# Kernel tuning notes

Hardware: AMD Instinct MI355X
Metric: run time of the kernel (lower is better)

The kernel has to match this reference:

```python
import jax, jax.numpy as jnp
import numpy as np

NEG_SLOPE = 0.2  # PyG GATConv default


def add_self_loops(edge_index, num_nodes):
    loops = jnp.arange(num_nodes, dtype=edge_index.dtype)
    return jnp.concatenate([edge_index, jnp.stack([loops, loops])], axis=1)


def gat_conv(x, edge_index, W, att_src, att_dst, bias, heads, out_ch, concat):
    # x: [N, F_in]; edge_index: [2, E] with row0=src(j), row1=dst(i)
    N = x.shape[0]
    xl = (x @ W).reshape(N, heads, out_ch)              # [N, H, C]
    src, dst = edge_index[0], edge_index[1]
    a_src = jnp.einsum('nhc,hc->nh', xl, att_src)        # [N, H]
    a_dst = jnp.einsum('nhc,hc->nh', xl, att_dst)        # [N, H]
    alpha = jax.nn.leaky_relu(a_src[src] + a_dst[dst], NEG_SLOPE)  # [E, H]
    # segment softmax over incoming edges of each dst node
    m = jax.ops.segment_max(alpha, dst, num_segments=N)  # [N, H]
    e = jnp.exp(alpha - m[dst])
    denom = jax.ops.segment_sum(e, dst, num_segments=N)
    coef = e / (denom[dst] + 1e-16)                      # [E, H]
    msg = xl[src] * coef[..., None]                      # [E, H, C]
    out = jax.ops.segment_sum(msg, dst, num_segments=N)  # [N, H, C]
    out = out.reshape(N, heads * out_ch) if concat else out.mean(axis=1)
    return out + bias


def setup_inputs() -> dict:
    key = jax.random.key(0)
    ks = jax.random.split(key, 12)
    N, E = 50000, 800000
    nfeat, nhid, nheads, nclass = 512, 8, 8, 16
    hid = nhid * nheads  # 64
    s1 = 1.0 / np.sqrt(nfeat)
    s2 = 1.0 / np.sqrt(hid)
    return {
        'x': jax.random.normal(ks[0], (N, nfeat), jnp.float32),
        'edge_index': jax.random.randint(ks[1], (2, E), 0, N, jnp.int64 if jax.config.jax_enable_x64 else jnp.int32),
        'W1': jax.random.uniform(ks[2], (nfeat, hid), jnp.float32, -s1, s1),
        'att_src1': jax.random.uniform(ks[3], (nheads, nhid), jnp.float32, -s2, s2),
        'att_dst1': jax.random.uniform(ks[4], (nheads, nhid), jnp.float32, -s2, s2),
        'bias1': jnp.zeros((hid,), jnp.float32),
        'W2': jax.random.uniform(ks[5], (hid, nclass), jnp.float32, -s2, s2),
        'att_src2': jax.random.uniform(ks[6], (1, nclass), jnp.float32, -0.25, 0.25),
        'att_dst2': jax.random.uniform(ks[7], (1, nclass), jnp.float32, -0.25, 0.25),
        'bias2': jnp.zeros((nclass,), jnp.float32),
    }


def reference(x, edge_index, W1, att_src1, att_dst1, bias1, W2, att_src2, att_dst2, bias2):
    N = x.shape[0]
    ei = add_self_loops(edge_index, N)
    # dropout layers are identity at inference
    h = gat_conv(x, ei, W1, att_src1, att_dst1, bias1, heads=8, out_ch=8, concat=True)
    o = gat_conv(h, ei, W2, att_src2, att_dst2, bias2, heads=1, out_ch=16, concat=True)
    o = jax.nn.elu(o)
    return jax.nn.log_softmax(o, axis=1)
```

## Files before the change

### kernel.cpp

```cpp
#include <hip/hip_runtime.h>
#include <math.h>

#define NEG_SLOPE 0.2f

typedef short short8 __attribute__((ext_vector_type(8)));
typedef float floatx4 __attribute__((ext_vector_type(4)));

static __device__ __forceinline__ float bf2f(unsigned short u) {
  return __uint_as_float(((unsigned int)u) << 16);
}
static __device__ __forceinline__ unsigned short f2bf(float f) {
  unsigned int u = __float_as_uint(f);
  u = (u + 0x7fffu + ((u >> 16) & 1u)) >> 16;
  return (unsigned short)u;
}

__global__ void init_misc(const float* __restrict__ W1, unsigned short* __restrict__ W1t,
                          int* __restrict__ deg, int N) {
  int b = blockIdx.x;
  if (b < 128) {
    int i = b * 256 + threadIdx.x;
    int k = i >> 6, c = i & 63;
    W1t[c * 512 + k] = f2bf(W1[i]);
  } else {
    int n = (b - 128) * 256 + threadIdx.x;
    if (n < N) deg[n] = 1;
  }
}

__global__ __launch_bounds__(256) void cvt_hist(const float* __restrict__ x,
                                                unsigned short* __restrict__ xb,
                                                const int* __restrict__ ei,
                                                int* __restrict__ deg,
                                                int* __restrict__ rank,
                                                long long total, int E, int ipc, int NH) {
  int b = blockIdx.x;
  int tid = threadIdx.x;
  if (b < NH) {
    int beg = b * ipc;
    int end = min(beg + ipc, E);
    for (int i = beg + tid; i < end; i += 256) {
      int d = ei[E + i];
      rank[i] = atomicAdd(&deg[d], 1);
    }
    return;
  }
  long long base = (long long)(b - NH) * 2048;
  long long i0 = base + tid * 4;
  long long i1 = base + 1024 + tid * 4;
  if (i1 + 4 <= total) {
    float4 f0 = *(const float4*)(x + i0);
    float4 f1 = *(const float4*)(x + i1);
    ushort4 u0 = make_ushort4(f2bf(f0.x), f2bf(f0.y), f2bf(f0.z), f2bf(f0.w));
    ushort4 u1 = make_ushort4(f2bf(f1.x), f2bf(f1.y), f2bf(f1.z), f2bf(f1.w));
    *(ushort4*)(xb + i0) = u0;
    *(ushort4*)(xb + i1) = u1;
  } else {
#pragma unroll
    for (int k = 0; k < 4; ++k) {
      if (i0 + k < total) xb[i0 + k] = f2bf(x[i0 + k]);
      if (i1 + k < total) xb[i1 + k] = f2bf(x[i1 + k]);
    }
  }
}

__global__ __launch_bounds__(256) void gemm1_scan(const unsigned short* __restrict__ xb,
                                                  const unsigned short* __restrict__ W1t,
                                                  const float* __restrict__ att_src,
                                                  const float* __restrict__ att_dst,
                                                  unsigned short* __restrict__ xlb,
                                                  float* __restrict__ a_src,
                                                  float* __restrict__ a_dst, int M,
                                                  const int* __restrict__ deg,
                                                  int* __restrict__ rowptr, int G1) {
  __shared__ unsigned short As[64 * 72];
  __shared__ unsigned short Bs[64 * 72];
  int tid = threadIdx.x;
  if ((int)blockIdx.x >= G1) {
    int* wsum = (int*)As;
    int lane = tid & 63, wv = tid >> 6;
    int carry = 0;
    for (int base = 0; base < M; base += 8192) {
      int i0 = base + tid * 32;
      int d[32];
      if (i0 + 32 <= M) {
#pragma unroll
        for (int g = 0; g < 8; ++g) {
          int4 a = *(const int4*)(deg + i0 + g * 4);
          d[g * 4] = a.x; d[g * 4 + 1] = a.y; d[g * 4 + 2] = a.z; d[g * 4 + 3] = a.w;
        }
      } else {
#pragma unroll
        for (int k = 0; k < 32; ++k) d[k] = (i0 + k < M) ? deg[i0 + k] : 0;
      }
      int e[32];
      e[0] = d[0];
#pragma unroll
      for (int k = 1; k < 32; ++k) e[k] = e[k - 1] + d[k];
      int tot = e[31];
      int v = tot;
#pragma unroll
      for (int off = 1; off < 64; off <<= 1) {
        int t = __shfl_up(v, off, 64);
        if (lane >= off) v += t;
      }
      if (lane == 63) wsum[wv] = v;
      __syncthreads();
      int woff = carry;
      for (int w = 0; w < wv; ++w) woff += wsum[w];
      int excl = woff + v - tot;
      int r[32];
      r[0] = excl;
#pragma unroll
      for (int k = 1; k < 32; ++k) r[k] = excl + e[k - 1];
      if (i0 + 32 <= M) {
#pragma unroll
        for (int g = 0; g < 8; ++g)
          *(int4*)(rowptr + i0 + g * 4) =
              make_int4(r[g * 4], r[g * 4 + 1], r[g * 4 + 2], r[g * 4 + 3]);
      } else {
#pragma unroll
        for (int k = 0; k < 32; ++k)
          if (i0 + k < M) rowptr[i0 + k] = r[k];
      }
      int bt = (wsum[0] + wsum[1]) + (wsum[2] + wsum[3]);
      __syncthreads();
      carry += bt;
    }
    if (tid == 0) rowptr[M] = carry;
    return;
  }
  int w = tid >> 6, lane = tid & 63;
  int q = lane >> 4, cl = lane & 15;
  int row0 = blockIdx.x << 6;
  floatx4 acc[4] = {};

  int sr = tid >> 2;
  int c4 = tid & 3;
  int arow = row0 + sr;
  bool okA = arow < M;
  const unsigned short* Ap = xb + (size_t)arow * 512;
  const unsigned short* Bp = W1t + sr * 512;
  unsigned short* AsW0 = As + sr * 72 + c4 * 8;
  unsigned short* BsW0 = Bs + sr * 72 + c4 * 8;

  uint4 a0 = make_uint4(0, 0, 0, 0), a1 = a0;
  uint4 b0, b1;
  if (okA) {
    a0 = *(const uint4*)(Ap + c4 * 8);
    a1 = *(const uint4*)(Ap + 32 + c4 * 8);
  }
  b0 = *(const uint4*)(Bp + c4 * 8);
  b1 = *(const uint4*)(Bp + 32 + c4 * 8);

#pragma unroll
  for (int k0 = 0; k0 < 512; k0 += 64) {
    __syncthreads();
    *(uint4*)(AsW0)      = a0;
    *(uint4*)(AsW0 + 32) = a1;
    *(uint4*)(BsW0)      = b0;
    *(uint4*)(BsW0 + 32) = b1;
    __syncthreads();
    if (k0 < 448) {
      a0 = make_uint4(0, 0, 0, 0); a1 = a0;
      if (okA) {
        a0 = *(const uint4*)(Ap + k0 + 64 + c4 * 8);
        a1 = *(const uint4*)(Ap + k0 + 96 + c4 * 8);
      }
      b0 = *(const uint4*)(Bp + k0 + 64 + c4 * 8);
      b1 = *(const uint4*)(Bp + k0 + 96 + c4 * 8);
    }
#pragma unroll
    for (int kk = 0; kk < 2; ++kk) {
      short8 af = *(const short8*)(As + (w * 16 + cl) * 72 + kk * 32 + q * 8);
#pragma unroll
      for (int t = 0; t < 4; ++t) {
        short8 bf = *(const short8*)(Bs + (t * 16 + cl) * 72 + kk * 32 + q * 8);
        acc[t] = __builtin_amdgcn_mfma_f32_16x16x32_bf16(af, bf, acc[t], 0, 0, 0);
      }
    }
  }

  float asv[4], adv[4];
#pragma unroll
  for (int t = 0; t < 4; ++t) {
    asv[t] = att_src[t * 16 + cl];
    adv[t] = att_dst[t * 16 + cl];
  }
#pragma unroll
  for (int reg = 0; reg < 4; ++reg) {
    int r = row0 + w * 16 + q * 4 + reg;
    bool ok = r < M;
#pragma unroll
    for (int t = 0; t < 4; ++t) {
      float v = acc[t][reg];
      if (ok) xlb[(size_t)r * 64 + t * 16 + cl] = f2bf(v);
      float ps = v * asv[t];
      float pd = v * adv[t];
      ps += __shfl_xor(ps, 1); pd += __shfl_xor(pd, 1);
      ps += __shfl_xor(ps, 2); pd += __shfl_xor(pd, 2);
      ps += __shfl_xor(ps, 4); pd += __shfl_xor(pd, 4);
      if (ok && (cl & 7) == 0) {
        int h = t * 2 + (cl >> 3);
        a_src[r * 8 + h] = ps;
        a_dst[r * 8 + h] = pd;
      }
    }
  }
}

__global__ __launch_bounds__(256) void scatter_rank(const int* __restrict__ ei,
                                                    const int* __restrict__ rank,
                                                    const int* __restrict__ rowptr,
                                                    int* __restrict__ srcs,
                                                    int E, int N, int ipc) {
  int slice = blockIdx.x & 7;
  int chunk = blockIdx.x >> 3;
  int lo = (int)(((long long)slice * N) >> 3);
  int hi = (int)(((long long)(slice + 1) * N) >> 3);
  int total = E + N;
  int beg = chunk * ipc;
  int end = min(beg + ipc, total);
  for (int i = beg + threadIdx.x; i < end; i += 256) {
    int d = (i < E) ? ei[E + i] : (i - E);
    if (d >= lo && d < hi) {
      int pos = rowptr[d] + ((i < E) ? rank[i] : 0);
      srcs[pos] = (i < E) ? ei[i] : d;
    }
  }
}

__global__ __launch_bounds__(256) void agg1_fused(const int* __restrict__ rowptr,
                                                  const int* __restrict__ srcs,
                                                  const float* __restrict__ a_src,
                                                  const float* __restrict__ a_dst,
                                                  const unsigned short* __restrict__ xlb,
                                                  const float* __restrict__ bias1,
                                                  const float* __restrict__ W2,
                                                  const float* __restrict__ att_src2,
                                                  const float* __restrict__ att_dst2,
                                                  float* __restrict__ xl2,
                                                  float* __restrict__ a_src2,
                                                  float* __restrict__ a_dst2, int N) {
  __shared__ float W2s[64 * 16];
  __shared__ float hsm[4][64];
  int tid = threadIdx.x;
  W2s[tid]       = W2[tid];
  W2s[tid + 256] = W2[tid + 256];
  W2s[tid + 512] = W2[tid + 512];
  W2s[tid + 768] = W2[tid + 768];
  __syncthreads();

  int wv = tid >> 6, lane = tid & 63;
  int node = (blockIdx.x << 2) + wv;
  if (node >= N) return;
  int half = lane >> 5;
  int j = lane & 31;
  int h = j >> 2;
  int beg = rowptr[node], end = rowptr[node + 1];
  float ad = a_dst[node * 8 + h];
  float den = 0.f, acc0 = 0.f, acc1 = 0.f;

  int p = beg + half;
  bool v0 = p < end,      v1 = p + 2 < end,  v2 = p + 4 < end,  v3 = p + 6 < end;
  bool v4 = p + 8 < end,  v5 = p + 10 < end, v6 = p + 12 < end, v7 = p + 14 < end;
  int s0 = srcs[v0 ? p : beg];
  int s1 = srcs[v1 ? p + 2 : beg];
  int s2 = srcs[v2 ? p + 4 : beg];
  int s3 = srcs[v3 ? p + 6 : beg];
  int s4 = srcs[v4 ? p + 8 : beg];
  int s5 = srcs[v5 ? p + 10 : beg];
  int s6 = srcs[v6 ? p + 12 : beg];
  int s7 = srcs[v7 ? p + 14 : beg];
  while (v0) {
    int np = p + 16;
    bool u0 = np < end,      u1 = np + 2 < end,  u2 = np + 4 < end,  u3 = np + 6 < end;
    bool u4 = np + 8 < end,  u5 = np + 10 < end, u6 = np + 12 < end, u7 = np + 14 < end;
    int t0 = srcs[u0 ? np : beg];
    int t1 = srcs[u1 ? np + 2 : beg];
    int t2 = srcs[u2 ? np + 4 : beg];
    int t3 = srcs[u3 ? np + 6 : beg];
    int t4 = srcs[u4 ? np + 8 : beg];
    int t5 = srcs[u5 ? np + 10 : beg];
    int t6 = srcs[u6 ? np + 12 : beg];
    int t7 = srcs[u7 ? np + 14 : beg];
    float a0 = a_src[s0 * 8 + h] + ad;
    float a1 = a_src[s1 * 8 + h] + ad;
    float a2 = a_src[s2 * 8 + h] + ad;
    float a3 = a_src[s3 * 8 + h] + ad;
    float a4 = a_src[s4 * 8 + h] + ad;
    float a5 = a_src[s5 * 8 + h] + ad;
    float a6 = a_src[s6 * 8 + h] + ad;
    float a7 = a_src[s7 * 8 + h] + ad;
    ushort2 x0 = *(const ushort2*)(xlb + (size_t)s0 * 64 + 2 * j);
    ushort2 x1 = *(const ushort2*)(xlb + (size_t)s1 * 64 + 2 * j);
    ushort2 x2 = *(const ushort2*)(xlb + (size_t)s2 * 64 + 2 * j);
    ushort2 x3 = *(const ushort2*)(xlb + (size_t)s3 * 64 + 2 * j);
    ushort2 x4 = *(const ushort2*)(xlb + (size_t)s4 * 64 + 2 * j);
    ushort2 x5 = *(const ushort2*)(xlb + (size_t)s5 * 64 + 2 * j);
    ushort2 x6 = *(const ushort2*)(xlb + (size_t)s6 * 64 + 2 * j);
    ushort2 x7 = *(const ushort2*)(xlb + (size_t)s7 * 64 + 2 * j);
    a0 = a0 >= 0.f ? a0 : NEG_SLOPE * a0;
    a1 = a1 >= 0.f ? a1 : NEG_SLOPE * a1;
    a2 = a2 >= 0.f ? a2 : NEG_SLOPE * a2;
    a3 = a3 >= 0.f ? a3 : NEG_SLOPE * a3;
    a4 = a4 >= 0.f ? a4 : NEG_SLOPE * a4;
    a5 = a5 >= 0.f ? a5 : NEG_SLOPE * a5;
    a6 = a6 >= 0.f ? a6 : NEG_SLOPE * a6;
    a7 = a7 >= 0.f ? a7 : NEG_SLOPE * a7;
    float w0 = v0 ? __expf(a0) : 0.f;
    float w1 = v1 ? __expf(a1) : 0.f;
    float w2 = v2 ? __expf(a2) : 0.f;
    float w3 = v3 ? __expf(a3) : 0.f;
    float w4 = v4 ? __expf(a4) : 0.f;
    float w5 = v5 ? __expf(a5) : 0.f;
    float w6 = v6 ? __expf(a6) : 0.f;
    float w7 = v7 ? __expf(a7) : 0.f;
    den += ((w0 + w1) + (w2 + w3)) + ((w4 + w5) + (w6 + w7));
    acc0 += (w0 * bf2f(x0.x) + w1 * bf2f(x1.x)) + (w2 * bf2f(x2.x) + w3 * bf2f(x3.x)) +
            (w4 * bf2f(x4.x) + w5 * bf2f(x5.x)) + (w6 * bf2f(x6.x) + w7 * bf2f(x7.x));
    acc1 += (w0 * bf2f(x0.y) + w1 * bf2f(x1.y)) + (w2 * bf2f(x2.y) + w3 * bf2f(x3.y)) +
            (w4 * bf2f(x4.y) + w5 * bf2f(x5.y)) + (w6 * bf2f(x6.y) + w7 * bf2f(x7.y));
    p = np;
    s0 = t0; s1 = t1; s2 = t2; s3 = t3; s4 = t4; s5 = t5; s6 = t6; s7 = t7;
    v0 = u0; v1 = u1; v2 = u2; v3 = u3; v4 = u4; v5 = u5; v6 = u6; v7 = u7;
  }
  den  += __shfl_xor(den, 32);
  acc0 += __shfl_xor(acc0, 32);
  acc1 += __shfl_xor(acc1, 32);
  float inv = 1.f / (den + 1e-16f);
  float2 bv = *(const float2*)(bias1 + 2 * j);
  float h0 = acc0 * inv + bv.x;
  float h1 = acc1 * inv + bv.y;
  if (half == 0) {
    hsm[wv][2 * j]     = h0;
    hsm[wv][2 * j + 1] = h1;
  }
  if (lane < 16) {
    float sum = 0.f;
#pragma unroll
    for (int k = 0; k < 64; ++k) sum += hsm[wv][k] * W2s[k * 16 + lane];
    xl2[(size_t)node * 16 + lane] = sum;
    float ps = sum * att_src2[lane];
    float pd = sum * att_dst2[lane];
#pragma unroll
    for (int w = 8; w >= 1; w >>= 1) {
      ps += __shfl_xor(ps, w, 16);
      pd += __shfl_xor(pd, w, 16);
    }
    if (lane == 0) { a_src2[node] = ps; a_dst2[node] = pd; }
  }
}

__global__ __launch_bounds__(256) void agg2_fin(const int* __restrict__ rowptr,
                                                const int* __restrict__ srcs,
                                                const float* __restrict__ a_src2,
                                                const float* __restrict__ a_dst2,
                                                const float* __restrict__ xl2,
                                                const float* __restrict__ bias2,
                                                float* __restrict__ out, int N) {
  int t = blockIdx.x * blockDim.x + threadIdx.x;
  int node = t >> 4;
  int c = t & 15;
  if (node >= N) return;
  int beg = rowptr[node], end = rowptr[node + 1];
  float ad = a_dst2[node];
  float den = 0.f, acc = 0.f;
  int p = beg;
  bool v0 = true,          v1 = p + 1 < end, v2 = p + 2 < end, v3 = p + 3 < end;
  bool v4 = p + 4 < end,   v5 = p + 5 < end, v6 = p + 6 < end, v7 = p + 7 < end;
  int s0 = srcs[p];
  int s1 = srcs[v1 ? p + 1 : beg];
  int s2 = srcs[v2 ? p + 2 : beg];
  int s3 = srcs[v3 ? p + 3 : beg];
  int s4 = srcs[v4 ? p + 4 : beg];
  int s5 = srcs[v5 ? p + 5 : beg];
  int s6 = srcs[v6 ? p + 6 : beg];
  int s7 = srcs[v7 ? p + 7 : beg];
  while (v0) {
    int np = p + 8;
    bool u0 = np < end,     u1 = np + 1 < end, u2 = np + 2 < end, u3 = np + 3 < end;
    bool u4 = np + 4 < end, u5 = np + 5 < end, u6 = np + 6 < end, u7 = np + 7 < end;
    int t0 = srcs[u0 ? np : beg];
    int t1 = srcs[u1 ? np + 1 : beg];
    int t2 = srcs[u2 ? np + 2 : beg];
    int t3 = srcs[u3 ? np + 3 : beg];
    int t4 = srcs[u4 ? np + 4 : beg];
    int t5 = srcs[u5 ? np + 5 : beg];
    int t6 = srcs[u6 ? np + 6 : beg];
    int t7 = srcs[u7 ? np + 7 : beg];
    float a0 = a_src2[s0] + ad, a1 = a_src2[s1] + ad;
    float a2 = a_src2[s2] + ad, a3 = a_src2[s3] + ad;
    float a4 = a_src2[s4] + ad, a5 = a_src2[s5] + ad;
    float a6 = a_src2[s6] + ad, a7 = a_src2[s7] + ad;
    float x0 = xl2[(size_t)s0 * 16 + c], x1 = xl2[(size_t)s1 * 16 + c];
    float x2 = xl2[(size_t)s2 * 16 + c], x3 = xl2[(size_t)s3 * 16 + c];
    float x4 = xl2[(size_t)s4 * 16 + c], x5 = xl2[(size_t)s5 * 16 + c];
    float x6 = xl2[(size_t)s6 * 16 + c], x7 = xl2[(size_t)s7 * 16 + c];
    a0 = a0 >= 0.f ? a0 : NEG_SLOPE * a0;
    a1 = a1 >= 0.f ? a1 : NEG_SLOPE * a1;
    a2 = a2 >= 0.f ? a2 : NEG_SLOPE * a2;
    a3 = a3 >= 0.f ? a3 : NEG_SLOPE * a3;
    a4 = a4 >= 0.f ? a4 : NEG_SLOPE * a4;
    a5 = a5 >= 0.f ? a5 : NEG_SLOPE * a5;
    a6 = a6 >= 0.f ? a6 : NEG_SLOPE * a6;
    a7 = a7 >= 0.f ? a7 : NEG_SLOPE * a7;
    float w0 = v0 ? __expf(a0) : 0.f;
    float w1 = v1 ? __expf(a1) : 0.f;
    float w2 = v2 ? __expf(a2) : 0.f;
    float w3 = v3 ? __expf(a3) : 0.f;
    float w4 = v4 ? __expf(a4) : 0.f;
    float w5 = v5 ? __expf(a5) : 0.f;
    float w6 = v6 ? __expf(a6) : 0.f;
    float w7 = v7 ? __expf(a7) : 0.f;
    den += ((w0 + w1) + (w2 + w3)) + ((w4 + w5) + (w6 + w7));
    acc += (w0 * x0 + w1 * x1) + (w2 * x2 + w3 * x3) +
           (w4 * x4 + w5 * x5) + (w6 * x6 + w7 * x7);
    p = np;
    s0 = t0; s1 = t1; s2 = t2; s3 = t3; s4 = t4; s5 = t5; s6 = t6; s7 = t7;
    v0 = u0; v1 = u1; v2 = u2; v3 = u3; v4 = u4; v5 = u5; v6 = u6; v7 = u7;
  }
  float o = acc / (den + 1e-16f) + bias2[c];
  o = o > 0.f ? o : expm1f(o);
  float mx = o;
#pragma unroll
  for (int w = 8; w >= 1; w >>= 1) mx = fmaxf(mx, __shfl_xor(mx, w, 16));
  float e = __expf(o - mx);
  float ssum = e;
#pragma unroll
  for (int w = 8; w >= 1; w >>= 1) ssum += __shfl_xor(ssum, w, 16);
  out[(size_t)node * 16 + c] = o - mx - logf(ssum);
}

static inline size_t rnd16(size_t x) { return (x + 15) & ~(size_t)15; }

extern "C" void kernel_launch(void* const* d_in, const int* in_sizes, int n_in,
                              void* d_out, int out_size, void* d_ws, size_t ws_size,
                              hipStream_t stream) {
  const float* x        = (const float*)d_in[0];
  const int*   ei       = (const int*)d_in[1];
  const float* W1       = (const float*)d_in[2];
  const float* att_src1 = (const float*)d_in[3];
  const float* att_dst1 = (const float*)d_in[4];
  const float* bias1    = (const float*)d_in[5];
  const float* W2       = (const float*)d_in[6];
  const float* att_src2 = (const float*)d_in[7];
  const float* att_dst2 = (const float*)d_in[8];
  const float* bias2    = (const float*)d_in[9];
  float* out = (float*)d_out;

  int N = in_sizes[0] / 512;
  int E = in_sizes[1] / 2;

  char* ws = (char*)d_ws;
  unsigned short* xb  = (unsigned short*)ws;  ws += rnd16((size_t)N * 512 * 2);
  unsigned short* xlb = (unsigned short*)ws;  ws += rnd16((size_t)N * 64 * 2);
  unsigned short* W1t = (unsigned short*)ws;  ws += rnd16((size_t)512 * 64 * 2);
  float* a_src1 = (float*)ws;                 ws += rnd16((size_t)N * 8 * 4);
  float* a_dst1 = (float*)ws;                 ws += rnd16((size_t)N * 8 * 4);
  float* xl2    = (float*)ws;                 ws += rnd16((size_t)N * 16 * 4);
  float* a_src2 = (float*)ws;                 ws += rnd16((size_t)N * 4);
  float* a_dst2 = (float*)ws;                 ws += rnd16((size_t)N * 4);
  int* deg      = (int*)ws;                   ws += rnd16((size_t)N * 4);
  int* rowptr   = (int*)ws;                   ws += rnd16((size_t)(N + 1) * 4);
  int* rank     = (int*)ws;                   ws += rnd16((size_t)E * 4);
  int* srcs     = (int*)ws;                   ws += rnd16((size_t)(E + N) * 4);

  const int NCHUNK = 256;
  const int NH = 256;
  long long total = (long long)N * 512;
  int GC = (int)((total + 2047) / 2048);
  int G1 = (N + 63) / 64;
  int ipc_h = (E + NH - 1) / NH;
  int ipc_s = (E + N + NCHUNK - 1) / NCHUNK;

  init_misc<<<128 + (N + 255) / 256, 256, 0, stream>>>(W1, W1t, deg, N);
  cvt_hist<<<NH + GC, 256, 0, stream>>>(x, xb, ei, deg, rank, total, E, ipc_h, NH);
  gemm1_scan<<<G1 + 1, 256, 0, stream>>>(xb, W1t, att_src1, att_dst1,
                                         xlb, a_src1, a_dst1, N, deg, rowptr, G1);
  scatter_rank<<<NCHUNK * 8, 256, 0, stream>>>(ei, rank, rowptr, srcs, E, N, ipc_s);
  agg1_fused<<<(N + 3) / 4, 256, 0, stream>>>(rowptr, srcs, a_src1, a_dst1, xlb,
                                              bias1, W2, att_src2, att_dst2,
                                              xl2, a_src2, a_dst2, N);
  agg2_fin<<<((size_t)N * 16 + 255) / 256, 256, 0, stream>>>(rowptr, srcs, a_src2, a_dst2,
                                                             xl2, bias2, out, N);
}
```

Before: 281.6 us.

## Fold W1 transpose into cvt_hist, memset counts, and flatten CSR scatter

Removes the init_misc launch. Degree counters are now zeroed with hipMemsetAsync, the self-loop +1 is added during the scan, and the W1 bf16 transpose is done by extra blocks inside cvt_hist. The CSR scatter no longer makes 8 passes over the edge list with destination-slice filtering. It is a single pass over 256 blocks, with the self-loop always placed first in each row. This removes redundant reads of the edge index but gives up the locality of sliced writes into srcs.

After: 292.3 us. 3.8% more time.

```diff
diff --git a/kernel.cpp b/kernel.cpp
--- a/kernel.cpp
+++ b/kernel.cpp
@@ -15,25 +15,15 @@
   return (unsigned short)u;
 }
 
-__global__ void init_misc(const float* __restrict__ W1, unsigned short* __restrict__ W1t,
-                          int* __restrict__ deg, int N) {
-  int b = blockIdx.x;
-  if (b < 128) {
-    int i = b * 256 + threadIdx.x;
-    int k = i >> 6, c = i & 63;
-    W1t[c * 512 + k] = f2bf(W1[i]);
-  } else {
-    int n = (b - 128) * 256 + threadIdx.x;
-    if (n < N) deg[n] = 1;
-  }
-}
-
 __global__ __launch_bounds__(256) void cvt_hist(const float* __restrict__ x,
                                                 unsigned short* __restrict__ xb,
+                                                const float* __restrict__ W1,
+                                                unsigned short* __restrict__ W1t,
                                                 const int* __restrict__ ei,
-                                                int* __restrict__ deg,
+                                                int* __restrict__ cnt,
                                                 int* __restrict__ rank,
-                                                long long total, int E, int ipc, int NH) {
+                                                long long total, int E,
+                                                int ipc, int NH) {
   int b = blockIdx.x;
   int tid = threadIdx.x;
   if (b < NH) {
@@ -41,11 +31,17 @@
     int end = min(beg + ipc, E);
     for (int i = beg + tid; i < end; i += 256) {
       int d = ei[E + i];
-      rank[i] = atomicAdd(&deg[d], 1);
+      rank[i] = atomicAdd(&cnt[d], 1);
     }
     return;
   }
-  long long base = (long long)(b - NH) * 2048;
+  if (b < NH + 128) {
+    int i = (b - NH) * 256 + tid;
+    int k = i >> 6, c = i & 63;
+    W1t[c * 512 + k] = f2bf(W1[i]);
+    return;
+  }
+  long long base = (long long)(b - NH - 128) * 2048;
   long long i0 = base + tid * 4;
   long long i1 = base + 1024 + tid * 4;
   if (i1 + 4 <= total) {
@@ -71,7 +67,7 @@
                                                   unsigned short* __restrict__ xlb,
                                                   float* __restrict__ a_src,
                                                   float* __restrict__ a_dst, int M,
-                                                  const int* __restrict__ deg,
+                                                  const int* __restrict__ cnt,
                                                   int* __restrict__ rowptr, int G1) {
   __shared__ unsigned short As[64 * 72];
   __shared__ unsigned short Bs[64 * 72];
@@ -86,12 +82,13 @@
       if (i0 + 32 <= M) {
 #pragma unroll
         for (int g = 0; g < 8; ++g) {
-          int4 a = *(const int4*)(deg + i0 + g * 4);
-          d[g * 4] = a.x; d[g * 4 + 1] = a.y; d[g * 4 + 2] = a.z; d[g * 4 + 3] = a.w;
+          int4 a = *(const int4*)(cnt + i0 + g * 4);
+          d[g * 4] = a.x + 1; d[g * 4 + 1] = a.y + 1;
+          d[g * 4 + 2] = a.z + 1; d[g * 4 + 3] = a.w + 1;
         }
       } else {
 #pragma unroll
-        for (int k = 0; k < 32; ++k) d[k] = (i0 + k < M) ? deg[i0 + k] : 0;
+        for (int k = 0; k < 32; ++k) d[k] = (i0 + k < M) ? (cnt[i0 + k] + 1) : 0;
       }
       int e[32];
       e[0] = d[0];
@@ -209,23 +206,21 @@
   }
 }
 
-__global__ __launch_bounds__(256) void scatter_rank(const int* __restrict__ ei,
+__global__ __launch_bounds__(256) void scatter_flat(const int* __restrict__ ei,
                                                     const int* __restrict__ rank,
                                                     const int* __restrict__ rowptr,
                                                     int* __restrict__ srcs,
                                                     int E, int N, int ipc) {
-  int slice = blockIdx.x & 7;
-  int chunk = blockIdx.x >> 3;
-  int lo = (int)(((long long)slice * N) >> 3);
-  int hi = (int)(((long long)(slice + 1) * N) >> 3);
   int total = E + N;
-  int beg = chunk * ipc;
+  int beg = blockIdx.x * ipc;
   int end = min(beg + ipc, total);
   for (int i = beg + threadIdx.x; i < end; i += 256) {
-    int d = (i < E) ? ei[E + i] : (i - E);
-    if (d >= lo && d < hi) {
-      int pos = rowptr[d] + ((i < E) ? rank[i] : 0);
-      srcs[pos] = (i < E) ? ei[i] : d;
+    if (i < E) {
+      int d = ei[E + i];
+      srcs[rowptr[d] + 1 + rank[i]] = ei[i];
+    } else {
+      int n = i - E;
+      srcs[rowptr[n]] = n;
     }
   }
 }
@@ -461,24 +456,25 @@
   float* xl2    = (float*)ws;                 ws += rnd16((size_t)N * 16 * 4);
   float* a_src2 = (float*)ws;                 ws += rnd16((size_t)N * 4);
   float* a_dst2 = (float*)ws;                 ws += rnd16((size_t)N * 4);
-  int* deg      = (int*)ws;                   ws += rnd16((size_t)N * 4);
+  int* cnt      = (int*)ws;                   ws += rnd16((size_t)N * 4);
   int* rowptr   = (int*)ws;                   ws += rnd16((size_t)(N + 1) * 4);
   int* rank     = (int*)ws;                   ws += rnd16((size_t)E * 4);
   int* srcs     = (int*)ws;                   ws += rnd16((size_t)(E + N) * 4);
 
-  const int NCHUNK = 256;
-  const int NH = 256;
+  const int NH  = 256;
+  const int NSC = 256;
   long long total = (long long)N * 512;
   int GC = (int)((total + 2047) / 2048);
   int G1 = (N + 63) / 64;
   int ipc_h = (E + NH - 1) / NH;
-  int ipc_s = (E + N + NCHUNK - 1) / NCHUNK;
-
-  init_misc<<<128 + (N + 255) / 256, 256, 0, stream>>>(W1, W1t, deg, N);
-  cvt_hist<<<NH + GC, 256, 0, stream>>>(x, xb, ei, deg, rank, total, E, ipc_h, NH);
+  int ipc_s = (E + N + NSC - 1) / NSC;
+
+  hipMemsetAsync(cnt, 0, (size_t)N * sizeof(int), stream);
+  cvt_hist<<<NH + 128 + GC, 256, 0, stream>>>(x, xb, W1, W1t, ei, cnt, rank,
+                                              total, E, ipc_h, NH);
   gemm1_scan<<<G1 + 1, 256, 0, stream>>>(xb, W1t, att_src1, att_dst1,
-                                         xlb, a_src1, a_dst1, N, deg, rowptr, G1);
-  scatter_rank<<<NCHUNK * 8, 256, 0, stream>>>(ei, rank, rowptr, srcs, E, N, ipc_s);
+                                         xlb, a_src1, a_dst1, N, cnt, rowptr, G1);
+  scatter_flat<<<NSC, 256, 0, stream>>>(ei, rank, rowptr, srcs, E, N, ipc_s);
   agg1_fused<<<(N + 3) / 4, 256, 0, stream>>>(rowptr, srcs, a_src1, a_dst1, xlb,
                                               bias1, W2, att_src2, att_dst2,
                                               xl2, a_src2, a_dst2, N);
```
